# Performance work log

Hardware: AMD Instinct MI355X
Metric: run time of the kernel (lower is better)

Reference implementation:

```python
import jax, jax.numpy as jnp
import numpy as np

EMBED_DIM = 768


def setup_inputs() -> dict:
    key = jax.random.key(0)
    k1, k2, k3, k4, k5 = jax.random.split(key, 5)
    C = EMBED_DIM
    B, N = 32, 1024
    s = 1.0 / np.sqrt(C)
    x = jax.random.normal(k1, (B, N, C), dtype=jnp.float32)
    qkv_w = jax.random.normal(k2, (C, 3 * C), dtype=jnp.float32) * s  # [in, out]
    qkv_b = jax.random.normal(k3, (3 * C,), dtype=jnp.float32) * 0.02
    proj_w = jax.random.normal(k4, (C, C), dtype=jnp.float32) * s
    proj_b = jax.random.normal(k5, (C,), dtype=jnp.float32) * 0.02
    return {"x": x, "qkv_w": qkv_w, "qkv_b": qkv_b, "proj_w": proj_w, "proj_b": proj_b}


def reference(x, qkv_w, qkv_b, proj_w, proj_b):
    B, N, C = x.shape
    qkv = (x @ qkv_w + qkv_b).reshape(B, N, 3, C)
    q, k, v = qkv[:, :, 0], qkv[:, :, 1], qkv[:, :, 2]  # each [B, N, C]
    # single-head full attention; scale by sqrt(C) as in source
    scores = jnp.einsum('bnc,bmc->bnm', q, k) / jnp.sqrt(jnp.asarray(C, x.dtype))
    attn = jax.nn.softmax(scores, axis=-1)  # dropout p=0.0 -> identity
    out = jnp.einsum('bnm,bmc->bnc', attn, v)
    # faithful to source: transpose(1,2).reshape(B,N,C) permutes the data
    out = jnp.swapaxes(out, 1, 2).reshape(B, N, C)
    return out @ proj_w + proj_b
```

## Files before the change

### kernel.cpp

```cpp
#include <hip/hip_runtime.h>
#include <hip/hip_bf16.h>


#define BM 256
#define BN 256
#define BKK 64

typedef __attribute__((ext_vector_type(8))) short bf16x8;
typedef __attribute__((ext_vector_type(4))) float f32x4;

__device__ __forceinline__ unsigned short f2b(float f) {
  unsigned int u = __float_as_uint(f);
  u = u + 0x7fffu + ((u >> 16) & 1u);
  return (unsigned short)(u >> 16);
}

__device__ __forceinline__ void g2l16(const void* g, void* l) {
  __builtin_amdgcn_global_load_lds(
      (const __attribute__((address_space(1))) unsigned int*)g,
      (__attribute__((address_space(3))) unsigned int*)l, 16, 0, 0);
}

template <int EPI>
__global__ __launch_bounds__(512, 2) void gemm_nt8(
    const unsigned short* __restrict__ A, const unsigned short* __restrict__ B,
    unsigned short* __restrict__ Cb, unsigned short* __restrict__ Ck,
    unsigned short* __restrict__ Cv, float* __restrict__ Cf,
    const float* __restrict__ bias, float* __restrict__ Z, int K, int lda,
    int ldb, int ldc, long bsA, long bsB, long bsC, float scale, int MT,
    int NN) {
  __shared__ unsigned short As[2][BM][BKK];
  __shared__ unsigned short Bs[2][BN][BKK];

  const int id = blockIdx.x;
  const int w = (id & 7) * ((int)gridDim.x >> 3) + (id >> 3);
  const int pb = MT * NN;
  const int bz = w / pb;
  const int r = w - bz * pb;
  const int bym = r / NN;
  const int bxn = r - bym * NN;

  const unsigned short* Ag = A + (long)bz * bsA + (long)(bym * BM) * lda;
  const unsigned short* Bg = B + (long)bz * bsB + (long)(bxn * BN) * ldb;

  const int tid = threadIdx.x;
  const int wave = tid >> 6;
  const int lane = tid & 63;
  const int l15 = lane & 15;
  const int lk = lane >> 4;
  const int wm = (wave >> 2) << 7;
  const int wn = (wave & 3) << 6;

  const int sr = lane >> 3;
  const int sc = (lane & 7) ^ sr;

  f32x4 acc[8][4];
#pragma unroll
  for (int m = 0; m < 8; ++m)
#pragma unroll
    for (int n = 0; n < 4; ++n)
#pragma unroll
      for (int p = 0; p < 4; ++p) acc[m][n][p] = 0.f;

  auto stA = [&](int d, int h, int k0) {
#pragma unroll
    for (int i = 0; i < 2; ++i) {
      const int rb = (h << 7) + (wave << 4) + (i << 3);
      g2l16(Ag + (long)(rb + sr) * lda + k0 + (sc << 3), &As[d][rb][0]);
    }
  };
  auto stB = [&](int d, int h, int k0) {
#pragma unroll
    for (int i = 0; i < 2; ++i) {
      const int rb = (h << 7) + (wave << 4) + (i << 3);
      g2l16(Bg + (long)(rb + sr) * ldb + k0 + (sc << 3), &Bs[d][rb][0]);
    }
  };
  auto ldA = [&](int d, int m, int ks) {
    return *(const bf16x8*)&As[d][wm + (m << 4) + l15]
                              [((((ks << 2) | lk) ^ (l15 & 7)) << 3)];
  };
  auto ldB = [&](int d, int n, int ks) {
    return *(const bf16x8*)&Bs[d][wn + (n << 4) + l15]
                              [((((ks << 2) | lk) ^ (l15 & 7)) << 3)];
  };

  const int NT = K / BKK;
  stA(0, 0, 0); stA(0, 1, 0); stB(0, 0, 0); stB(0, 1, 0);
  stA(1, 0, BKK); stA(1, 1, BKK); stB(1, 0, BKK); stB(1, 1, BKK);
  asm volatile("s_waitcnt vmcnt(8)" ::: "memory");
  __builtin_amdgcn_sched_barrier(0);
  __builtin_amdgcn_s_barrier();

  int cur = 0;
  for (int t = 0; t < NT; ++t) {
    const int nxt = cur ^ 1;
    const bool st2 = (t + 2 < NT);
    const int k2 = (t + 2) * BKK;

    bf16x8 aL[4][2], bA[2][2];
#pragma unroll
    for (int m = 0; m < 4; ++m)
#pragma unroll
      for (int ks = 0; ks < 2; ++ks) aL[m][ks] = ldA(cur, m, ks);
#pragma unroll
    for (int n = 0; n < 2; ++n)
#pragma unroll
      for (int ks = 0; ks < 2; ++ks) bA[n][ks] = ldB(cur, n, ks);
    __builtin_amdgcn_s_barrier();
    asm volatile("s_waitcnt lgkmcnt(0)" ::: "memory");
    __builtin_amdgcn_sched_barrier(0);
    __builtin_amdgcn_s_setprio(1);
#pragma unroll
    for (int m = 0; m < 4; ++m)
#pragma unroll
      for (int n = 0; n < 2; ++n)
#pragma unroll
        for (int ks = 0; ks < 2; ++ks)
          acc[m][n] = __builtin_amdgcn_mfma_f32_16x16x32_bf16(
              aL[m][ks], bA[n][ks], acc[m][n], 0, 0, 0);
    __builtin_amdgcn_s_setprio(0);
    __builtin_amdgcn_s_barrier();

    bf16x8 bB[2][2];
#pragma unroll
    for (int n = 0; n < 2; ++n)
#pragma unroll
      for (int ks = 0; ks < 2; ++ks) bB[n][ks] = ldB(cur, n + 2, ks);
    __builtin_amdgcn_s_barrier();
    asm volatile("s_waitcnt lgkmcnt(0)" ::: "memory");
    __builtin_amdgcn_sched_barrier(0);
    __builtin_amdgcn_s_setprio(1);
#pragma unroll
    for (int m = 0; m < 4; ++m)
#pragma unroll
      for (int n = 0; n < 2; ++n)
#pragma unroll
        for (int ks = 0; ks < 2; ++ks)
          acc[m][n + 2] = __builtin_amdgcn_mfma_f32_16x16x32_bf16(
              aL[m][ks], bB[n][ks], acc[m][n + 2], 0, 0, 0);
    __builtin_amdgcn_s_setprio(0);
    __builtin_amdgcn_s_barrier();

    bf16x8 aH[4][2];
#pragma unroll
    for (int m = 0; m < 4; ++m)
#pragma unroll
      for (int ks = 0; ks < 2; ++ks) aH[m][ks] = ldA(cur, m + 4, ks);
    if (st2) { stB(cur, 0, k2); stB(cur, 1, k2); }
    __builtin_amdgcn_s_barrier();
    asm volatile("s_waitcnt lgkmcnt(0)" ::: "memory");
    __builtin_amdgcn_sched_barrier(0);
    __builtin_amdgcn_s_setprio(1);
#pragma unroll
    for (int m = 0; m < 4; ++m)
#pragma unroll
      for (int n = 0; n < 2; ++n)
#pragma unroll
        for (int ks = 0; ks < 2; ++ks)
          acc[m + 4][n] = __builtin_amdgcn_mfma_f32_16x16x32_bf16(
              aH[m][ks], bA[n][ks], acc[m + 4][n], 0, 0, 0);
    __builtin_amdgcn_s_setprio(0);
    __builtin_amdgcn_s_barrier();

    if (st2) { stA(cur, 0, k2); stA(cur, 1, k2); }
    __builtin_amdgcn_s_setprio(1);
#pragma unroll
    for (int m = 0; m < 4; ++m)
#pragma unroll
      for (int n = 0; n < 2; ++n)
#pragma unroll
        for (int ks = 0; ks < 2; ++ks)
          acc[m + 4][n + 2] = __builtin_amdgcn_mfma_f32_16x16x32_bf16(
              aH[m][ks], bB[n][ks], acc[m + 4][n + 2], 0, 0, 0);
    __builtin_amdgcn_s_setprio(0);
    if (st2)
      asm volatile("s_waitcnt vmcnt(8)" ::: "memory");
    else
      asm volatile("s_waitcnt vmcnt(0)" ::: "memory");
    __builtin_amdgcn_sched_barrier(0);
    __builtin_amdgcn_s_barrier();
    cur = nxt;
  }

  const int row0 = bym * BM + wm + (lk << 2);
  const int col0 = bxn * BN + wn;

  if constexpr (EPI == 1) {
    const int seg = (bxn * BN) / 768;
    unsigned short* O = (seg == 0) ? Cb : ((seg == 1) ? Ck : Cv);
    float bv[4];
#pragma unroll
    for (int n = 0; n < 4; ++n) bv[n] = bias[col0 + (n << 4) + l15];
    const int cl0 = col0 + l15 - seg * 768;
#pragma unroll
    for (int m = 0; m < 8; ++m)
#pragma unroll
      for (int p = 0; p < 4; ++p) {
        const long rr = row0 + (m << 4) + p;
#pragma unroll
        for (int n = 0; n < 4; ++n)
          O[rr * 768 + cl0 + (n << 4)] = f2b(acc[m][n][p] + bv[n]);
      }
  } else if constexpr (EPI == 2) {
    float bv[4];
#pragma unroll
    for (int n = 0; n < 4; ++n) bv[n] = bias[col0 + (n << 4) + l15];
#pragma unroll
    for (int m = 0; m < 8; ++m)
#pragma unroll
      for (int p = 0; p < 4; ++p) {
        const long rr = row0 + (m << 4) + p;
#pragma unroll
        for (int n = 0; n < 4; ++n)
          Cf[rr * ldc + col0 + (n << 4) + l15] = acc[m][n][p] + bv[n];
      }
  } else if constexpr (EPI == 3) {
    unsigned short* C = Cb + (long)bz * bsC;
#pragma unroll
    for (int m = 0; m < 8; ++m) {
      float es[4] = {0.f, 0.f, 0.f, 0.f};
#pragma unroll
      for (int p = 0; p < 4; ++p) {
        const long rr = row0 + (m << 4) + p;
#pragma unroll
        for (int n = 0; n < 4; ++n) {
          const float e = __expf(acc[m][n][p] * scale);
          es[p] += e;
          C[rr * ldc + col0 + (n << 4) + l15] = f2b(e);
        }
      }
#pragma unroll
      for (int p = 0; p < 4; ++p) {
        float s = es[p];
        s += __shfl_xor(s, 1);
        s += __shfl_xor(s, 2);
        s += __shfl_xor(s, 4);
        s += __shfl_xor(s, 8);
        if (l15 == 0)
          atomicAdd(&Z[(long)bz * 1024 + row0 + (m << 4) + p], s);
      }
    }
  } else {
    unsigned short* C = Cb + (long)bz * bsC;
    float zv[4];
#pragma unroll
    for (int n = 0; n < 4; ++n)
      zv[n] = 1.f / Z[(long)bz * 1024 + col0 + (n << 4) + l15];
#pragma unroll
    for (int m = 0; m < 8; ++m)
#pragma unroll
      for (int p = 0; p < 4; ++p) {
        const long rr = row0 + (m << 4) + p;
#pragma unroll
        for (int n = 0; n < 4; ++n)
          C[rr * ldc + col0 + (n << 4) + l15] = f2b(acc[m][n][p] * zv[n]);
      }
  }
}

__global__ __launch_bounds__(256) void prep(
    const float4* __restrict__ x, ushort4* __restrict__ x_bf,
    const float* __restrict__ qkv_w, unsigned short* __restrict__ Wqkv,
    const float* __restrict__ proj_w, unsigned short* __restrict__ Wp) {
  const int blk = blockIdx.x;
  if (blk < 24576) {
    const long i = (long)blk * 256 + threadIdx.x;
    float4 f = x[i];
    ushort4 o;
    o.x = f2b(f.x); o.y = f2b(f.y); o.z = f2b(f.z); o.w = f2b(f.w);
    x_bf[i] = o;
  } else if (blk < 24576 + 6912) {
    const long i = (long)(blk - 24576) * 256 + threadIdx.x;
    const int k = (int)(i % 768);
    const int j = (int)(i / 768);
    Wqkv[i] = f2b(qkv_w[(long)k * 2304 + j]);
  } else {
    const long i = (long)(blk - 24576 - 6912) * 256 + threadIdx.x;
    const int k = (int)(i % 768);
    const int j = (int)(i / 768);
    Wp[i] = f2b(proj_w[(long)k * 768 + j]);
  }
}

__global__ __launch_bounds__(256) void transpose_v(
    const unsigned short* __restrict__ V, unsigned short* __restrict__ Vt) {
  __shared__ unsigned short T[64][72];
  const int b = blockIdx.z;
  const int d0 = blockIdx.x << 6;
  const int m0 = blockIdx.y << 6;
  const unsigned short* Vb = V + (long)b * 786432;
  unsigned short* Vtb = Vt + (long)b * 786432;
  const int tid = threadIdx.x;
  const int r = tid >> 2;
  const int c4 = tid & 3;
#pragma unroll
  for (int h = 0; h < 2; ++h) {
    const int cc = (c4 + (h << 2)) << 3;
    *(uint4*)&T[r][cc] = *(const uint4*)&Vb[(long)(m0 + r) * 768 + d0 + cc];
  }
  __syncthreads();
#pragma unroll
  for (int h = 0; h < 2; ++h) {
    const int mm = (c4 + (h << 2)) << 3;
    alignas(16) unsigned short tmp[8];
#pragma unroll
    for (int e = 0; e < 8; ++e) tmp[e] = T[mm + e][r];
    *(uint4*)&Vtb[(long)(d0 + r) * 1024 + m0 + mm] = *(uint4*)tmp;
  }
}

extern "C" void kernel_launch(void* const* d_in, const int* in_sizes, int n_in,
                              void* d_out, int out_size, void* d_ws,
                              size_t ws_size, hipStream_t stream) {
  const float* x = (const float*)d_in[0];
  const float* qkv_w = (const float*)d_in[1];
  const float* qkv_b = (const float*)d_in[2];
  const float* proj_w = (const float*)d_in[3];
  const float* proj_b = (const float*)d_in[4];
  float* out = (float*)d_out;

  char* ws = (char*)d_ws;
  unsigned short* x_bf = (unsigned short*)ws;
  unsigned short* Wqkv = (unsigned short*)(ws + 50331648);
  unsigned short* Wp = (unsigned short*)(ws + 53870592);
  unsigned short* Qb = (unsigned short*)(ws + 55050240);
  unsigned short* Kb = (unsigned short*)(ws + 105381888);
  unsigned short* Vb = (unsigned short*)(ws + 155713536);
  unsigned short* Sb = (unsigned short*)(ws + 206045184);
  unsigned short* Vt = x_bf;
  unsigned short* Hb = Qb;
  float* Zs = (float*)Vb;

  prep<<<33792, 256, 0, stream>>>((const float4*)x, (ushort4*)x_bf, qkv_w,
                                  Wqkv, proj_w, Wp);

  gemm_nt8<1><<<1152, 512, 0, stream>>>(
      x_bf, Wqkv, Qb, Kb, Vb, nullptr, qkv_b, nullptr, 768, 768, 768, 0, 0, 0,
      0, 1.f, 128, 9);

  transpose_v<<<dim3(12, 16, 32), 256, 0, stream>>>(Vb, Vt);

  hipMemsetAsync(Zs, 0, 32 * 1024 * sizeof(float), stream);

  gemm_nt8<3><<<512, 512, 0, stream>>>(
      Qb, Kb, Sb, nullptr, nullptr, nullptr, nullptr, Zs, 768, 768, 768, 1024,
      786432, 786432, 1048576, 0.03608439182435161f, 4, 4);

  gemm_nt8<4><<<384, 512, 0, stream>>>(
      Vt, Sb, Hb, nullptr, nullptr, nullptr, nullptr, Zs, 1024, 1024, 1024,
      1024, 786432, 1048576, 786432, 1.f, 3, 4);

  gemm_nt8<2><<<384, 512, 0, stream>>>(
      Hb, Wp, nullptr, nullptr, nullptr, out, proj_b, nullptr, 768, 768, 768,
      768, 0, 0, 0, 1.f, 128, 3);
}
```

Before: 549.5 us.

## Simplify GEMM main loop to two phases with single barrier before refill

```diff
diff --git a/kernel.cpp b/kernel.cpp
--- a/kernel.cpp
+++ b/kernel.cpp
@@ -91,96 +91,65 @@
   asm volatile("s_waitcnt vmcnt(8)" ::: "memory");
   __builtin_amdgcn_sched_barrier(0);
   __builtin_amdgcn_s_barrier();
+  __builtin_amdgcn_sched_barrier(0);
 
   int cur = 0;
   for (int t = 0; t < NT; ++t) {
-    const int nxt = cur ^ 1;
     const bool st2 = (t + 2 < NT);
     const int k2 = (t + 2) * BKK;
 
-    bf16x8 aL[4][2], bA[2][2];
+    bf16x8 bv[4][2], aL[4][2];
+#pragma unroll
+    for (int n = 0; n < 4; ++n)
+#pragma unroll
+      for (int ks = 0; ks < 2; ++ks) bv[n][ks] = ldB(cur, n, ks);
 #pragma unroll
     for (int m = 0; m < 4; ++m)
 #pragma unroll
       for (int ks = 0; ks < 2; ++ks) aL[m][ks] = ldA(cur, m, ks);
-#pragma unroll
-    for (int n = 0; n < 2; ++n)
-#pragma unroll
-      for (int ks = 0; ks < 2; ++ks) bA[n][ks] = ldB(cur, n, ks);
-    __builtin_amdgcn_s_barrier();
-    asm volatile("s_waitcnt lgkmcnt(0)" ::: "memory");
-    __builtin_amdgcn_sched_barrier(0);
+
     __builtin_amdgcn_s_setprio(1);
 #pragma unroll
     for (int m = 0; m < 4; ++m)
 #pragma unroll
-      for (int n = 0; n < 2; ++n)
+      for (int n = 0; n < 4; ++n)
 #pragma unroll
         for (int ks = 0; ks < 2; ++ks)
           acc[m][n] = __builtin_amdgcn_mfma_f32_16x16x32_bf16(
-              aL[m][ks], bA[n][ks], acc[m][n], 0, 0, 0);
+              aL[m][ks], bv[n][ks], acc[m][n], 0, 0, 0);
     __builtin_amdgcn_s_setprio(0);
-    __builtin_amdgcn_s_barrier();
-
-    bf16x8 bB[2][2];
-#pragma unroll
-    for (int n = 0; n < 2; ++n)
-#pragma unroll
-      for (int ks = 0; ks < 2; ++ks) bB[n][ks] = ldB(cur, n + 2, ks);
-    __builtin_amdgcn_s_barrier();
-    asm volatile("s_waitcnt lgkmcnt(0)" ::: "memory");
-    __builtin_amdgcn_sched_barrier(0);
+
+    bf16x8 aH[4][2];
+#pragma unroll
+    for (int m = 0; m < 4; ++m)
+#pragma unroll
+      for (int ks = 0; ks < 2; ++ks) aH[m][ks] = ldA(cur, m + 4, ks);
+
     __builtin_amdgcn_s_setprio(1);
 #pragma unroll
     for (int m = 0; m < 4; ++m)
 #pragma unroll
-      for (int n = 0; n < 2; ++n)
-#pragma unroll
-        for (int ks = 0; ks < 2; ++ks)
-          acc[m][n + 2] = __builtin_amdgcn_mfma_f32_16x16x32_bf16(
-              aL[m][ks], bB[n][ks], acc[m][n + 2], 0, 0, 0);
-    __builtin_amdgcn_s_setprio(0);
-    __builtin_amdgcn_s_barrier();
-
-    bf16x8 aH[4][2];
-#pragma unroll
-    for (int m = 0; m < 4; ++m)
-#pragma unroll
-      for (int ks = 0; ks < 2; ++ks) aH[m][ks] = ldA(cur, m + 4, ks);
-    if (st2) { stB(cur, 0, k2); stB(cur, 1, k2); }
-    __builtin_amdgcn_s_barrier();
-    asm volatile("s_waitcnt lgkmcnt(0)" ::: "memory");
-    __builtin_amdgcn_sched_barrier(0);
-    __builtin_amdgcn_s_setprio(1);
-#pragma unroll
-    for (int m = 0; m < 4; ++m)
-#pragma unroll
-      for (int n = 0; n < 2; ++n)
+      for (int n = 0; n < 4; ++n)
 #pragma unroll
         for (int ks = 0; ks < 2; ++ks)
           acc[m + 4][n] = __builtin_amdgcn_mfma_f32_16x16x32_bf16(
-              aH[m][ks], bA[n][ks], acc[m + 4][n], 0, 0, 0);
+              aH[m][ks], bv[n][ks], acc[m + 4][n], 0, 0, 0);
     __builtin_amdgcn_s_setprio(0);
+
     __builtin_amdgcn_s_barrier();
-
-    if (st2) { stA(cur, 0, k2); stA(cur, 1, k2); }
-    __builtin_amdgcn_s_setprio(1);
-#pragma unroll
-    for (int m = 0; m < 4; ++m)
-#pragma unroll
-      for (int n = 0; n < 2; ++n)
-#pragma unroll
-        for (int ks = 0; ks < 2; ++ks)
-          acc[m + 4][n + 2] = __builtin_amdgcn_mfma_f32_16x16x32_bf16(
-              aH[m][ks], bB[n][ks], acc[m + 4][n + 2], 0, 0, 0);
-    __builtin_amdgcn_s_setprio(0);
+    __builtin_amdgcn_sched_barrier(0);
+    if (st2) {
+      stB(cur, 0, k2); stB(cur, 1, k2);
+      stA(cur, 0, k2); stA(cur, 1, k2);
+    }
     if (st2)
       asm volatile("s_waitcnt vmcnt(8)" ::: "memory");
     else
       asm volatile("s_waitcnt vmcnt(0)" ::: "memory");
     __builtin_amdgcn_sched_barrier(0);
     __builtin_amdgcn_s_barrier();
-    cur = nxt;
+    __builtin_amdgcn_sched_barrier(0);
+    cur ^= 1;
   }
 
   const int row0 = bym * BM + wm + (lk << 2);
@@ -189,9 +158,9 @@
   if constexpr (EPI == 1) {
     const int seg = (bxn * BN) / 768;
     unsigned short* O = (seg == 0) ? Cb : ((seg == 1) ? Ck : Cv);
-    float bv[4];
-#pragma unroll
-    for (int n = 0; n < 4; ++n) bv[n] = bias[col0 + (n << 4) + l15];
+    float bv2[4];
+#pragma unroll
+    for (int n = 0; n < 4; ++n) bv2[n] = bias[col0 + (n << 4) + l15];
     const int cl0 = col0 + l15 - seg * 768;
 #pragma unroll
     for (int m = 0; m < 8; ++m)
@@ -200,12 +169,12 @@
         const long rr = row0 + (m << 4) + p;
 #pragma unroll
         for (int n = 0; n < 4; ++n)
-          O[rr * 768 + cl0 + (n << 4)] = f2b(acc[m][n][p] + bv[n]);
+          O[rr * 768 + cl0 + (n << 4)] = f2b(acc[m][n][p] + bv2[n]);
       }
   } else if constexpr (EPI == 2) {
-    float bv[4];
-#pragma unroll
-    for (int n = 0; n < 4; ++n) bv[n] = bias[col0 + (n << 4) + l15];
+    float bv2[4];
+#pragma unroll
+    for (int n = 0; n < 4; ++n) bv2[n] = bias[col0 + (n << 4) + l15];
 #pragma unroll
     for (int m = 0; m < 8; ++m)
 #pragma unroll
@@ -213,7 +182,7 @@
         const long rr = row0 + (m << 4) + p;
 #pragma unroll
         for (int n = 0; n < 4; ++n)
-          Cf[rr * ldc + col0 + (n << 4) + l15] = acc[m][n][p] + bv[n];
+          Cf[rr * ldc + col0 + (n << 4) + l15] = acc[m][n][p] + bv2[n];
       }
   } else if constexpr (EPI == 3) {
     unsigned short* C = Cb + (long)bz * bsC;
```

Measured after the change: 559.3 us. About the same (+1.8%).
